# Kernel optimization log

Hardware: AMD Instinct MI355X
Metric: run time of the kernel (lower is better)

## Reference

```python
import jax, jax.numpy as jnp
import numpy as np

N = 100000      # nodes
E = 1600000     # edges per layer (avg degree 16)
F_IN = 128      # input features
H = 64          # hidden_layer
OUT = 32        # hidden_layer // 2
NEG_SLOPE = 0.2


def gat_layer(x, W, att_src, att_dst, b, edge_index):
    # PyG GATConv, heads=1, shared lin for src/dst (int in_channels)
    h = x @ W                                   # [N, H]
    a_src = (h * att_src).sum(-1)               # [N]
    a_dst = (h * att_dst).sum(-1)               # [N]
    src, dst = edge_index[0], edge_index[1]
    e = jax.nn.leaky_relu(a_src[src] + a_dst[dst], NEG_SLOPE)  # [E]
    # segment softmax over destination nodes
    m = jax.ops.segment_max(e, dst, num_segments=N)
    ex = jnp.exp(e - m[dst])
    s = jax.ops.segment_sum(ex, dst, num_segments=N)
    alpha = ex / (s[dst] + 1e-16)               # [E]
    out = jax.ops.segment_sum(h[src] * alpha[:, None], dst, num_segments=N)
    return out + b


def setup_inputs() -> dict:
    key = jax.random.key(0)
    ks = jax.random.split(key, 12)
    sc1 = 1.0 / np.sqrt(F_IN)
    sc2 = 1.0 / np.sqrt(H)
    return {
        "x": jax.random.normal(ks[0], (N, F_IN), jnp.float32),
        "edge_index1": jax.random.randint(ks[1], (2, E), 0, N, jnp.int64 if jax.config.jax_enable_x64 else jnp.int32),
        "edge_index2": jax.random.randint(ks[2], (2, E), 0, N, jnp.int64 if jax.config.jax_enable_x64 else jnp.int32),
        "W1": jax.random.normal(ks[3], (F_IN, H), jnp.float32) * sc1,
        "att_src1": jax.random.normal(ks[4], (H,), jnp.float32) * sc2,
        "att_dst1": jax.random.normal(ks[5], (H,), jnp.float32) * sc2,
        "b1": jnp.zeros((H,), jnp.float32),
        "W2": jax.random.normal(ks[6], (H, H), jnp.float32) * sc2,
        "att_src2": jax.random.normal(ks[7], (H,), jnp.float32) * sc2,
        "att_dst2": jax.random.normal(ks[8], (H,), jnp.float32) * sc2,
        "b2": jnp.zeros((H,), jnp.float32),
        "Wlin": jax.random.normal(ks[9], (H, OUT), jnp.float32) * sc2,
        "blin": jnp.zeros((OUT,), jnp.float32),
    }


def reference(x, edge_index1, edge_index2, W1, att_src1, att_dst1, b1,
              W2, att_src2, att_dst2, b2, Wlin, blin):
    h = gat_layer(x, W1, att_src1, att_dst1, b1, edge_index1)
    h = jax.nn.relu(h)                           # dropout p=0 -> identity
    h = gat_layer(h, W2, att_src2, att_dst2, b2, edge_index2)
    h = h @ Wlin + blin                          # [N, 32]
    return jax.nn.log_softmax(h, axis=1)         # SSL=False => deg_pred=0 omitted
```

## Files before the change

kernel.cpp:

```cpp
#include <hip/hip_runtime.h>
#include <math.h>

#define NEG_SLOPE 0.2f
#define NXCD 8
#define SUBCAP 8960

template <int K>
__global__ __launch_bounds__(256) void gemm_tile(
    const float* __restrict__ X, const float* __restrict__ W,
    const float* __restrict__ att_s, const float* __restrict__ att_d,
    float* __restrict__ H, float* __restrict__ As, float* __restrict__ Ad,
    int n)
{
    constexpr int XP = K + 4;
    constexpr int BK = 64;
    __shared__ float Xs[64 * XP];
    __shared__ float Ws[BK * 64];

    const int tid = threadIdx.x;
    const int node0 = blockIdx.x * 64;

    for (int i4 = tid; i4 < 64 * (K / 4); i4 += 256) {
        int r = i4 / (K / 4);
        int c = (i4 % (K / 4)) * 4;
        int nd = node0 + r;
        float4 v = make_float4(0.f, 0.f, 0.f, 0.f);
        if (nd < n) v = *(const float4*)&X[(size_t)nd * K + c];
        *(float4*)&Xs[r * XP + c] = v;
    }

    const int tx = tid & 15;
    const int ty = tid >> 4;

    float acc[4][4];
#pragma unroll
    for (int r = 0; r < 4; ++r)
#pragma unroll
        for (int f = 0; f < 4; ++f) acc[r][f] = 0.0f;

    for (int kc = 0; kc < K; kc += BK) {
        __syncthreads();
        for (int i = tid; i < BK * 64; i += 256) Ws[i] = W[kc * 64 + i];
        __syncthreads();

        for (int k = 0; k < BK; k += 4) {
            float4 a0 = *(const float4*)&Xs[(ty * 4 + 0) * XP + kc + k];
            float4 a1 = *(const float4*)&Xs[(ty * 4 + 1) * XP + kc + k];
            float4 a2 = *(const float4*)&Xs[(ty * 4 + 2) * XP + kc + k];
            float4 a3 = *(const float4*)&Xs[(ty * 4 + 3) * XP + kc + k];
            float4 b0 = *(const float4*)&Ws[(k + 0) * 64 + tx * 4];
            float4 b1 = *(const float4*)&Ws[(k + 1) * 64 + tx * 4];
            float4 b2 = *(const float4*)&Ws[(k + 2) * 64 + tx * 4];
            float4 b3 = *(const float4*)&Ws[(k + 3) * 64 + tx * 4];
#define GEMM_ROW(rr, av)                                                     \
            acc[rr][0] = fmaf(av.x, b0.x, acc[rr][0]);                       \
            acc[rr][1] = fmaf(av.x, b0.y, acc[rr][1]);                       \
            acc[rr][2] = fmaf(av.x, b0.z, acc[rr][2]);                       \
            acc[rr][3] = fmaf(av.x, b0.w, acc[rr][3]);                       \
            acc[rr][0] = fmaf(av.y, b1.x, acc[rr][0]);                       \
            acc[rr][1] = fmaf(av.y, b1.y, acc[rr][1]);                       \
            acc[rr][2] = fmaf(av.y, b1.z, acc[rr][2]);                       \
            acc[rr][3] = fmaf(av.y, b1.w, acc[rr][3]);                       \
            acc[rr][0] = fmaf(av.z, b2.x, acc[rr][0]);                       \
            acc[rr][1] = fmaf(av.z, b2.y, acc[rr][1]);                       \
            acc[rr][2] = fmaf(av.z, b2.z, acc[rr][2]);                       \
            acc[rr][3] = fmaf(av.z, b2.w, acc[rr][3]);                       \
            acc[rr][0] = fmaf(av.w, b3.x, acc[rr][0]);                       \
            acc[rr][1] = fmaf(av.w, b3.y, acc[rr][1]);                       \
            acc[rr][2] = fmaf(av.w, b3.z, acc[rr][2]);                       \
            acc[rr][3] = fmaf(av.w, b3.w, acc[rr][3]);
            GEMM_ROW(0, a0)
            GEMM_ROW(1, a1)
            GEMM_ROW(2, a2)
            GEMM_ROW(3, a3)
#undef GEMM_ROW
        }
    }

    float4 ats = *(const float4*)&att_s[tx * 4];
    float4 atd = *(const float4*)&att_d[tx * 4];
#pragma unroll
    for (int rr = 0; rr < 4; ++rr) {
        int nd = node0 + ty * 4 + rr;
        float vs = acc[rr][0] * ats.x + acc[rr][1] * ats.y +
                   acc[rr][2] * ats.z + acc[rr][3] * ats.w;
        float vd = acc[rr][0] * atd.x + acc[rr][1] * atd.y +
                   acc[rr][2] * atd.z + acc[rr][3] * atd.w;
#pragma unroll
        for (int off = 8; off; off >>= 1) {
            vs += __shfl_xor(vs, off);
            vd += __shfl_xor(vd, off);
        }
        if (nd < n) {
            float4 hv = make_float4(acc[rr][0], acc[rr][1], acc[rr][2], acc[rr][3]);
            *(float4*)&H[(size_t)nd * 64 + tx * 4] = hv;
            if (tx == 0) { As[nd] = vs; Ad[nd] = vd; }
        }
    }
}

__global__ __launch_bounds__(256) void fbucket_kernel(
    const int* __restrict__ src, const int* __restrict__ dst, int e,
    int* __restrict__ gcnt , unsigned* __restrict__ bkt)
{
    __shared__ int cnt[256];
    __shared__ int off[256];
    const int tid = threadIdx.x;
    const int chunk = (e + gridDim.x - 1) / gridDim.x;
    const int beg = blockIdx.x * chunk;
    const int end = min(beg + chunk, e);

    cnt[tid] = 0;
    __syncthreads();

    for (int i = beg + tid; i < end; i += 256)
        atomicAdd(&cnt[dst[i] >> 9], 1);
    __syncthreads();

    {
        int c = cnt[tid];
        off[tid] = tid * SUBCAP + (c ? atomicAdd(&gcnt[tid * 16], c) : 0);
    }
    __syncthreads();

    for (int i = beg + tid; i < end; i += 256) {
        int d = dst[i];
        int s = src[i];
        int sub = d >> 9;
        int pos = atomicAdd(&off[sub], 1);
        if (pos < (sub + 1) * SUBCAP)
            bkt[pos] = ((unsigned)(d & 511) << 17) | (unsigned)s;
    }
}

__global__ __launch_bounds__(256) void sort3_kernel(
    const unsigned* __restrict__ bkt, const int* __restrict__ gcnt,
    const float* __restrict__ As, const float* __restrict__ Ad,
    int2* __restrict__ rec, int2* __restrict__ rpBE, int n)
{
    __shared__ unsigned recs[SUBCAP];
    __shared__ int hist[512];
    __shared__ float AdS[512];
    __shared__ int sh[256];

    const int b = blockIdx.x;
    const int tid = threadIdx.x;
    const int base = b * SUBCAP;
    const int cnt = min(gcnt[b * 16], SUBCAP);

    for (int t = tid; t < 512; t += 256) {
        hist[t] = 0;
        int d = (b << 9) + t;
        AdS[t] = (d < n) ? Ad[d] : 0.0f;
    }
    __syncthreads();

    for (int i = tid; i < cnt; i += 256) {
        unsigned v = bkt[base + i];
        recs[i] = v;
        atomicAdd(&hist[v >> 17], 1);
    }
    __syncthreads();

    int a0 = hist[2 * tid];
    int a1 = hist[2 * tid + 1];
    sh[tid] = a0 + a1;
    __syncthreads();
    for (int off = 1; off < 256; off <<= 1) {
        int x = (tid >= off) ? sh[tid - off] : 0;
        __syncthreads();
        sh[tid] += x;
        __syncthreads();
    }
    int ex = (tid > 0) ? sh[tid - 1] : 0;
    hist[2 * tid]     = ex;
    hist[2 * tid + 1] = ex + a0;
    {
        int d0 = (b << 9) + 2 * tid;
        if (d0 < n)     rpBE[d0]     = make_int2(base + ex,          base + ex + a0);
        if (d0 + 1 < n) rpBE[d0 + 1] = make_int2(base + ex + a0,     base + ex + a0 + a1);
    }
    __syncthreads();

    for (int i = tid; i < cnt; i += 256) {
        unsigned v = recs[i];
        int dl = (int)(v >> 17);
        int s  = (int)(v & 0x1FFFFu);
        int pos = atomicAdd(&hist[dl], 1);
        float ev = As[s] + AdS[dl];
        ev = (ev >= 0.0f) ? ev : NEG_SLOPE * ev;
        rec[base + pos] = make_int2(s, __float_as_int(ev));
    }
}

__global__ __launch_bounds__(256) void aggr_kernel(
    const int2* __restrict__ rpBE, const int2* __restrict__ rec,
    const float* __restrict__ Hin, const float* __restrict__ bias,
    float* __restrict__ Out, int n, int lo_div, int relu_flag)
{
    const int lane = threadIdx.x & 63;
    const int wv = threadIdx.x >> 6;
    const float b = bias[lane];

    const int g = blockIdx.x & (NXCD - 1);
    const int gi = blockIdx.x >> 3;
    const int ngb = gridDim.x >> 3;
    const int lo = g * lo_div;
    const int hi = min(lo + lo_div, n);

    for (int d = lo + gi * 4 + wv; d < hi; d += ngb * 4) {
        const int2 be = rpBE[d];
        const int beg = be.x, end = be.y;

        float m = -1e30f, s = 0.0f;
        for (int i = beg + lane; i < end; i += 64) {
            float e = __int_as_float(rec[i].y);
            float mn = fmaxf(m, e);
            s = s * __expf(m - mn) + __expf(e - mn);
            m = mn;
        }
#pragma unroll
        for (int off = 32; off; off >>= 1) {
            float mo = __shfl_xor(m, off);
            float so = __shfl_xor(s, off);
            float mn = fmaxf(m, mo);
            s = s * __expf(m - mn) + so * __expf(mo - mn);
            m = mn;
        }
        const float inv = 1.0f / (s + 1e-16f);

        float acc0 = 0.f, acc1 = 0.f, acc2 = 0.f, acc3 = 0.f;
        int i = beg;
        for (; i + 4 <= end; i += 4) {
            int2 r0 = rec[i + 0];
            int2 r1 = rec[i + 1];
            int2 r2 = rec[i + 2];
            int2 r3 = rec[i + 3];
            float w0 = __expf(__int_as_float(r0.y) - m) * inv;
            float w1 = __expf(__int_as_float(r1.y) - m) * inv;
            float w2 = __expf(__int_as_float(r2.y) - m) * inv;
            float w3 = __expf(__int_as_float(r3.y) - m) * inv;
            acc0 = fmaf(w0, Hin[(size_t)r0.x * 64 + lane], acc0);
            acc1 = fmaf(w1, Hin[(size_t)r1.x * 64 + lane], acc1);
            acc2 = fmaf(w2, Hin[(size_t)r2.x * 64 + lane], acc2);
            acc3 = fmaf(w3, Hin[(size_t)r3.x * 64 + lane], acc3);
        }
        for (; i < end; ++i) {
            int2 r = rec[i];
            float w = __expf(__int_as_float(r.y) - m) * inv;
            acc0 = fmaf(w, Hin[(size_t)r.x * 64 + lane], acc0);
        }

        float r = (acc0 + acc1) + (acc2 + acc3) + b;
        if (relu_flag) r = fmaxf(r, 0.0f);
        Out[(size_t)d * 64 + lane] = r;
    }
}

__global__ __launch_bounds__(256) void lin_lsm_kernel(
    const float* __restrict__ Z, const float* __restrict__ Wl,
    const float* __restrict__ bl, float* __restrict__ out, int n)
{
    __shared__ float Ws[64 * 32];
    __shared__ float bs[32];
    for (int i = threadIdx.x; i < 64 * 32; i += 256) Ws[i] = Wl[i];
    if (threadIdx.x < 32) bs[threadIdx.x] = bl[threadIdx.x];
    __syncthreads();

    const int lane = threadIdx.x & 63;
    const int wv = threadIdx.x >> 6;
    const int half = lane >> 5;
    const int o = lane & 31;

    for (int base = (blockIdx.x * 4 + wv) * 2; base < n; base += gridDim.x * 8) {
        const int nd = base + half;
        float acc = 0.0f;
        if (nd < n) {
            const float* z = Z + (size_t)nd * 64;
#pragma unroll
            for (int k = 0; k < 64; ++k)
                acc = fmaf(z[k], Ws[k * 32 + o], acc);
            acc += bs[o];
        }
        float m = acc;
#pragma unroll
        for (int off = 16; off; off >>= 1) m = fmaxf(m, __shfl_xor(m, off, 32));
        float ex = __expf(acc - m);
        float s = ex;
#pragma unroll
        for (int off = 16; off; off >>= 1) s += __shfl_xor(s, off, 32);
        if (nd < n) out[(size_t)nd * 32 + o] = acc - m - logf(s);
    }
}

extern "C" void kernel_launch(void* const* d_in, const int* in_sizes, int n_in,
                              void* d_out, int out_size, void* d_ws, size_t ws_size,
                              hipStream_t stream)
{
    const float* x        = (const float*)d_in[0];
    const int*   ei1      = (const int*)d_in[1];
    const int*   ei2      = (const int*)d_in[2];
    const float* W1       = (const float*)d_in[3];
    const float* att_src1 = (const float*)d_in[4];
    const float* att_dst1 = (const float*)d_in[5];
    const float* b1       = (const float*)d_in[6];
    const float* W2       = (const float*)d_in[7];
    const float* att_src2 = (const float*)d_in[8];
    const float* att_dst2 = (const float*)d_in[9];
    const float* b2       = (const float*)d_in[10];
    const float* Wlin     = (const float*)d_in[11];
    const float* blin     = (const float*)d_in[12];
    float* out = (float*)d_out;

    const int n = in_sizes[0] / 128;
    const int e = in_sizes[1] / 2;
    const int nsub = (n + 511) >> 9;

    size_t off = 0;
    auto alloc = [&](size_t bytes) {
        void* p = (char*)d_ws + off;
        off += (bytes + 255) & ~(size_t)255;
        return p;
    };
    float* bufH  = (float*)alloc((size_t)n * 64 * 4);
    float* bufZ  = (float*)alloc((size_t)n * 64 * 4);
    float* As    = (float*)alloc((size_t)n * 4);
    float* Ad    = (float*)alloc((size_t)n * 4);
    int2* rpBE   = (int2*)alloc((size_t)n * 8);
    int* gcnt    = (int*)alloc((size_t)256 * 16 * 4);
    int2* rec    = (int2*)alloc((size_t)nsub * SUBCAP * 8);

    unsigned* bkt = (unsigned*)bufZ;

    const int lo_div = (n + NXCD - 1) / NXCD;
    const int gTile = (n + 63) / 64;
    const int gAggr = NXCD * ((lo_div + 3) / 4);
    const int gBkt  = 512;

    gemm_tile<128><<<gTile, 256, 0, stream>>>(x, W1, att_src1, att_dst1, bufH, As, Ad, n);

    hipMemsetAsync(gcnt, 0, (size_t)256 * 16 * 4, stream);
    fbucket_kernel<<<gBkt, 256, 0, stream>>>(ei1, ei1 + e, e, gcnt, bkt);
    sort3_kernel<<<nsub, 256, 0, stream>>>(bkt, gcnt, As, Ad, rec, rpBE, n);
    aggr_kernel<<<gAggr, 256, 0, stream>>>(rpBE, rec, bufH, b1, bufZ, n, lo_div, 1);

    gemm_tile<64><<<gTile, 256, 0, stream>>>(bufZ, W2, att_src2, att_dst2, bufH, As, Ad, n);

    hipMemsetAsync(gcnt, 0, (size_t)256 * 16 * 4, stream);
    fbucket_kernel<<<gBkt, 256, 0, stream>>>(ei2, ei2 + e, e, gcnt, bkt);
    sort3_kernel<<<nsub, 256, 0, stream>>>(bkt, gcnt, As, Ad, rec, rpBE, n);
    aggr_kernel<<<gAggr, 256, 0, stream>>>(rpBE, rec, bufH, b2, bufZ, n, lo_div, 0);

    const int gLSM = (n + 7) / 8;
    lin_lsm_kernel<<<gLSM, 256, 0, stream>>>(bufZ, Wlin, blin, out, n);
}
```

Measured before the change: 480.0 us.

## Process four destination nodes per wavefront with float4 gathers in aggregation

Measured after the change: 455.7 us. 1.05x faster.

```diff
diff --git a/kernel.cpp b/kernel.cpp
--- a/kernel.cpp
+++ b/kernel.cpp
@@ -200,7 +200,12 @@
 {
     const int lane = threadIdx.x & 63;
     const int wv = threadIdx.x >> 6;
-    const float b = bias[lane];
+    const int grp = lane >> 4;
+    const int l16 = lane & 15;
+    const int gbase = grp << 4;
+
+    const float4 b4 = *(const float4*)&bias[l16 * 4];
+    const float bsc = bias[lane];
 
     const int g = blockIdx.x & (NXCD - 1);
     const int gi = blockIdx.x >> 3;
@@ -208,52 +213,136 @@
     const int lo = g * lo_div;
     const int hi = min(lo + lo_div, n);
 
-    for (int d = lo + gi * 4 + wv; d < hi; d += ngb * 4) {
-        const int2 be = rpBE[d];
-        const int beg = be.x, end = be.y;
-
-        float m = -1e30f, s = 0.0f;
-        for (int i = beg + lane; i < end; i += 64) {
-            float e = __int_as_float(rec[i].y);
-            float mn = fmaxf(m, e);
-            s = s * __expf(m - mn) + __expf(e - mn);
-            m = mn;
-        }
-#pragma unroll
-        for (int off = 32; off; off >>= 1) {
-            float mo = __shfl_xor(m, off);
-            float so = __shfl_xor(s, off);
-            float mn = fmaxf(m, mo);
-            s = s * __expf(m - mn) + so * __expf(mo - mn);
-            m = mn;
-        }
-        const float inv = 1.0f / (s + 1e-16f);
-
-        float acc0 = 0.f, acc1 = 0.f, acc2 = 0.f, acc3 = 0.f;
-        int i = beg;
-        for (; i + 4 <= end; i += 4) {
-            int2 r0 = rec[i + 0];
-            int2 r1 = rec[i + 1];
-            int2 r2 = rec[i + 2];
-            int2 r3 = rec[i + 3];
-            float w0 = __expf(__int_as_float(r0.y) - m) * inv;
-            float w1 = __expf(__int_as_float(r1.y) - m) * inv;
-            float w2 = __expf(__int_as_float(r2.y) - m) * inv;
-            float w3 = __expf(__int_as_float(r3.y) - m) * inv;
-            acc0 = fmaf(w0, Hin[(size_t)r0.x * 64 + lane], acc0);
-            acc1 = fmaf(w1, Hin[(size_t)r1.x * 64 + lane], acc1);
-            acc2 = fmaf(w2, Hin[(size_t)r2.x * 64 + lane], acc2);
-            acc3 = fmaf(w3, Hin[(size_t)r3.x * 64 + lane], acc3);
-        }
-        for (; i < end; ++i) {
-            int2 r = rec[i];
-            float w = __expf(__int_as_float(r.y) - m) * inv;
-            acc0 = fmaf(w, Hin[(size_t)r.x * 64 + lane], acc0);
-        }
-
-        float r = (acc0 + acc1) + (acc2 + acc3) + b;
-        if (relu_flag) r = fmaxf(r, 0.0f);
-        Out[(size_t)d * 64 + lane] = r;
+    for (int dbase = lo + gi * 16; dbase < hi; dbase += ngb * 16) {
+        const int d = dbase + wv * 4 + grp;
+        int beg = 0, deg = 0;
+        if (d < hi) {
+            int2 be = rpBE[d];
+            beg = be.x;
+            deg = be.y - be.x;
+        }
+
+        if (!__any(deg > 64)) {
+            int   sj[4];
+            float wj[4];
+            float m = -1e30f;
+#pragma unroll
+            for (int j = 0; j < 4; ++j) {
+                int idx = j * 16 + l16;
+                sj[j] = 0;
+                wj[j] = -1e30f;
+                if (idx < deg) {
+                    int2 rc = rec[beg + idx];
+                    sj[j] = rc.x;
+                    wj[j] = __int_as_float(rc.y);
+                }
+                m = fmaxf(m, wj[j]);
+            }
+#pragma unroll
+            for (int off = 8; off; off >>= 1) m = fmaxf(m, __shfl_xor(m, off));
+
+            float s = 0.0f;
+#pragma unroll
+            for (int j = 0; j < 4; ++j) {
+                float e = __expf(wj[j] - m);
+                e = (j * 16 + l16 < deg) ? e : 0.0f;
+                wj[j] = e;
+                s += e;
+            }
+#pragma unroll
+            for (int off = 8; off; off >>= 1) s += __shfl_xor(s, off);
+            const float inv = 1.0f / (s + 1e-16f);
+
+            int Tw = deg;
+#pragma unroll
+            for (int off = 32; off; off >>= 1) Tw = max(Tw, __shfl_xor(Tw, off));
+
+            float4 accA = make_float4(0.f, 0.f, 0.f, 0.f);
+            float4 accB = make_float4(0.f, 0.f, 0.f, 0.f);
+#pragma unroll
+            for (int j = 0; j < 4; ++j) {
+                if (Tw > j * 16) {
+#pragma unroll
+                    for (int i = 0; i < 16; i += 2) {
+                        int   s0 = __shfl(sj[j], gbase + i);
+                        float w0 = __shfl(wj[j], gbase + i);
+                        int   s1 = __shfl(sj[j], gbase + i + 1);
+                        float w1 = __shfl(wj[j], gbase + i + 1);
+                        float4 h0 = *(const float4*)&Hin[(size_t)s0 * 64 + l16 * 4];
+                        float4 h1 = *(const float4*)&Hin[(size_t)s1 * 64 + l16 * 4];
+                        accA.x = fmaf(w0, h0.x, accA.x);
+                        accA.y = fmaf(w0, h0.y, accA.y);
+                        accA.z = fmaf(w0, h0.z, accA.z);
+                        accA.w = fmaf(w0, h0.w, accA.w);
+                        accB.x = fmaf(w1, h1.x, accB.x);
+                        accB.y = fmaf(w1, h1.y, accB.y);
+                        accB.z = fmaf(w1, h1.z, accB.z);
+                        accB.w = fmaf(w1, h1.w, accB.w);
+                    }
+                }
+            }
+
+            if (d < hi) {
+                float4 r;
+                r.x = (accA.x + accB.x) * inv + b4.x;
+                r.y = (accA.y + accB.y) * inv + b4.y;
+                r.z = (accA.z + accB.z) * inv + b4.z;
+                r.w = (accA.w + accB.w) * inv + b4.w;
+                if (relu_flag) {
+                    r.x = fmaxf(r.x, 0.0f);
+                    r.y = fmaxf(r.y, 0.0f);
+                    r.z = fmaxf(r.z, 0.0f);
+                    r.w = fmaxf(r.w, 0.0f);
+                }
+                *(float4*)&Out[(size_t)d * 64 + l16 * 4] = r;
+            }
+        } else {
+#pragma unroll
+            for (int j = 0; j < 4; ++j) {
+                const int dd = __shfl(d, j * 16);
+                const int valid = __shfl((d < hi) ? 1 : 0, j * 16);
+                if (!valid) continue;
+                const int bj = __shfl(beg, j * 16);
+                const int dj = __shfl(deg, j * 16);
+                const int end = bj + dj;
+
+                float m = -1e30f, s = 0.0f;
+                for (int i = bj + lane; i < end; i += 64) {
+                    float e = __int_as_float(rec[i].y);
+                    float mn = fmaxf(m, e);
+                    s = s * __expf(m - mn) + __expf(e - mn);
+                    m = mn;
+                }
+#pragma unroll
+                for (int off = 32; off; off >>= 1) {
+                    float mo = __shfl_xor(m, off);
+                    float so = __shfl_xor(s, off);
+                    float mn = fmaxf(m, mo);
+                    s = s * __expf(m - mn) + so * __expf(mo - mn);
+                    m = mn;
+                }
+                const float inv = 1.0f / (s + 1e-16f);
+
+                float a0 = 0.f, a1 = 0.f;
+                int i = bj;
+                for (; i + 2 <= end; i += 2) {
+                    int2 r0 = rec[i + 0];
+                    int2 r1 = rec[i + 1];
+                    float w0 = __expf(__int_as_float(r0.y) - m) * inv;
+                    float w1 = __expf(__int_as_float(r1.y) - m) * inv;
+                    a0 = fmaf(w0, Hin[(size_t)r0.x * 64 + lane], a0);
+                    a1 = fmaf(w1, Hin[(size_t)r1.x * 64 + lane], a1);
+                }
+                for (; i < end; ++i) {
+                    int2 rr = rec[i];
+                    float w = __expf(__int_as_float(rr.y) - m) * inv;
+                    a0 = fmaf(w, Hin[(size_t)rr.x * 64 + lane], a0);
+                }
+                float r = a0 + a1 + bsc;
+                if (relu_flag) r = fmaxf(r, 0.0f);
+                Out[(size_t)dd * 64 + lane] = r;
+            }
+        }
     }
 }
 
@@ -334,7 +423,7 @@
 
     const int lo_div = (n + NXCD - 1) / NXCD;
     const int gTile = (n + 63) / 64;
-    const int gAggr = NXCD * ((lo_div + 3) / 4);
+    const int gAggr = NXCD * ((lo_div + 15) / 16);
     const int gBkt  = 512;
 
     gemm_tile<128><<<gTile, 256, 0, stream>>>(x, W1, att_src1, att_dst1, bufH, As, Ad, n);
```
